# Performance work log

Measured on AMD Instinct MI355X. Metric: run time of the kernel, lower is better.

Reference implementation:

```python
import jax, jax.numpy as jnp
import numpy as np

T = 16000        # signal length
N1 = 120         # first-order filters (J=12, Q=10)
NPSI2 = 14       # second-order filterbank size (Q2=1)
NPAIR = 553      # second-order coefficients -> 120 + 553 = 673 channels
SUB1 = 8         # subsample U1 before order 2
T2 = T // SUB1   # 2000
STR1 = 1000      # lowpass stride at length T  -> 16 output samples
STR2 = T2 // (T // STR1)  # 125 -> 16 output samples
LOG_EPS = 1e-6
BN_EPS = 1e-5


def _gauss_hat(N, xi, sigma):
    om = np.arange(N) / N
    return np.exp(-((om - xi) ** 2) / (2.0 * sigma ** 2)).astype(np.float32)


def _filterbank():
    Q = 10.0
    xi1 = 0.45 * 2.0 ** (-np.arange(N1) / Q)
    sig1 = np.maximum(xi1 * 0.1, 2.0 / T)
    psi1 = np.stack([_gauss_hat(T, x, s) for x, s in zip(xi1, sig1)])
    phi1 = _gauss_hat(T, 0.0, 0.4 / STR1)
    xi2 = 0.45 * 2.0 ** (-np.arange(NPSI2, dtype=np.float64))
    sig2 = np.maximum(xi2 * 0.2, 2.0 / T2)
    psi2 = np.stack([_gauss_hat(T2, x, s) for x, s in zip(xi2, sig2)])
    phi2 = _gauss_hat(T2, 0.0, 0.4 / STR2)
    pairs = [(i, j) for i in range(N1) for j in range(NPSI2) if xi2[j] < xi1[i] / 2.0]
    pairs = pairs[:NPAIR]
    assert len(pairs) == NPAIR
    pi1 = np.array([p[0] for p in pairs], np.int32)
    pi2 = np.array([p[1] for p in pairs], np.int32)
    return psi1, phi1, psi2, phi2, pi1, pi2


def setup_inputs():
    key = jax.random.key(0)
    ks = jax.random.split(key, 8)
    psi1, phi1, psi2, phi2, pi1, pi2 = _filterbank()
    B = 32
    inp = {
        "x": jax.random.normal(ks[0], (B, 1, T), jnp.float32),
        "psi1_hat": jnp.asarray(psi1),
        "phi1_hat": jnp.asarray(phi1),
        "psi2_hat": jnp.asarray(psi2),
        "phi2_hat": jnp.asarray(phi2),
        "gamma": jnp.ones((673,), jnp.float32),
        "beta": jnp.zeros((673,), jnp.float32),
        "W1": jax.random.normal(ks[1], (300, 673), jnp.float32) * 0.04,
        "b1": jnp.zeros((300,), jnp.float32),
        "W2": jax.random.normal(ks[2], (90, 300), jnp.float32) * 0.06,
        "b2": jnp.zeros((90,), jnp.float32),
        "W3": jax.random.normal(ks[3], (35, 90), jnp.float32) * 0.1,
        "b3": jnp.zeros((35,), jnp.float32),
        "pair_i1": jnp.asarray(pi1),
        "pair_i2": jnp.asarray(pi2),
    }
    return inp


def reference(x, psi1_hat, phi1_hat, psi2_hat, phi2_hat, gamma, beta,
              W1, b1, W2, b2, W3, b3, pair_i1, pair_i2):
    xs = x.squeeze(1)                                       # [B, T]
    Xf = jnp.fft.fft(xs)                                    # [B, T] c64
    # --- order 1: wavelet conv (freq-domain), modulus ---
    U1 = jnp.abs(jnp.fft.ifft(Xf[:, None, :] * psi1_hat[None]))        # [B, N1, T]
    # S1 = lowpass(U1) subsampled to 16 samples
    S1 = jnp.real(jnp.fft.ifft(jnp.fft.fft(U1) * phi1_hat))[..., ::STR1]  # [B, N1, 16]
    # --- order 2 on subsampled U1 ---
    U1sf = jnp.fft.fft(U1[..., ::SUB1])                     # [B, N1, T2]
    U2 = jnp.abs(jnp.fft.ifft(U1sf[:, pair_i1, :] * psi2_hat[pair_i2]))  # [B, NPAIR, T2]
    S2 = jnp.real(jnp.fft.ifft(jnp.fft.fft(U2) * phi2_hat))[..., ::STR2]  # [B, NPAIR, 16]
    S = jnp.concatenate([S1, S2], axis=1)                   # [B, 673, 16]
    # log-abs + temporal mean pooling
    f = jnp.mean(jnp.log(jnp.abs(S) + LOG_EPS), axis=-1)    # [B, 673]
    # BatchNorm1d (training mode: batch statistics)
    mu = jnp.mean(f, axis=0)
    var = jnp.var(f, axis=0)
    f = (f - mu) / jnp.sqrt(var + BN_EPS) * gamma + beta
    # MLP head
    h = jax.nn.relu(f @ W1.T + b1)
    h = jax.nn.relu(h @ W2.T + b2)
    return jax.nn.log_softmax(h @ W3.T + b3, axis=-1)
```

## Files before the change

### kernel.cpp

```cpp
#include <hip/hip_runtime.h>
#include <math.h>

typedef float2 cf;

__device__ __forceinline__ cf cadd(cf a, cf b){ return make_float2(a.x+b.x, a.y+b.y); }
__device__ __forceinline__ cf csub(cf a, cf b){ return make_float2(a.x-b.x, a.y-b.y); }
__device__ __forceinline__ cf cmul(cf a, cf b){ return make_float2(a.x*b.x - a.y*b.y, a.x*b.y + a.y*b.x); }

__device__ __forceinline__ int SW(int i){ return i ^ ((i>>4)&15); }
#define AT(x) s[SW(x)]
#define WFENCE asm volatile("" ::: "memory")

template<bool WAVE> __device__ __forceinline__ void SYf(){
  if constexpr (WAVE) { WFENCE; } else __syncthreads();
}

__device__ __forceinline__ int devB(int i){
  int jm = i/10 + 2;
  double kc = 900.0*exp2((double)(-jm));
  double sg = fmax(180.0*exp2((double)(-jm)), 2.0);
  return min(2000, (int)ceil(kc + 6.5*sg) + 1);
}

template<int N, int L, bool INV>
__device__ __forceinline__ void stage_r2(cf* __restrict__ s, const cf* __restrict__ tw, int tid, int nt){
  constexpr int Ls = L/2, nbf = N/2, tws = 16000/L;
  for (int q = tid; q < nbf; q += nt){
    int blk = q / Ls, j = q - blk*Ls;
    int base = blk*L + j;
    cf w1 = tw[tws*j]; if (INV) w1.y = -w1.y;
    if (!INV){
      cf a = AT(base), b = AT(base+Ls);
      AT(base) = cadd(a,b);
      AT(base+Ls) = cmul(csub(a,b), w1);
    } else {
      cf a = AT(base), b = cmul(AT(base+Ls), w1);
      AT(base) = cadd(a,b);
      AT(base+Ls) = csub(a,b);
    }
  }
}

template<int N, int L, bool INV>
__device__ __forceinline__ void stage_r4(cf* __restrict__ s, const cf* __restrict__ tw, int tid, int nt){
  constexpr int Ls = L/4, nbf = N/4, tws = 16000/L;
  for (int q = tid; q < nbf; q += nt){
    int blk = q / Ls, j = q - blk*Ls;
    int base = blk*L + j;
    cf w1 = tw[tws*j]; if (INV) w1.y = -w1.y;
    cf w2 = cmul(w1,w1), w3 = cmul(w2,w1);
    if (!INV){
      cf y0=AT(base), y1=AT(base+Ls), y2=AT(base+2*Ls), y3=AT(base+3*Ls);
      cf t0=cadd(y0,y2), t1=csub(y0,y2), t2=cadd(y1,y3), t3=csub(y1,y3);
      AT(base)      = cadd(t0,t2);
      AT(base+Ls)   = cmul(make_float2(t1.x + t3.y, t1.y - t3.x), w1);
      AT(base+2*Ls) = cmul(csub(t0,t2), w2);
      AT(base+3*Ls) = cmul(make_float2(t1.x - t3.y, t1.y + t3.x), w3);
    } else {
      cf z0=AT(base);
      cf z1=cmul(AT(base+Ls),   w1);
      cf z2=cmul(AT(base+2*Ls), w2);
      cf z3=cmul(AT(base+3*Ls), w3);
      cf t0=cadd(z0,z2), t1=csub(z0,z2), t2=cadd(z1,z3), t3=csub(z1,z3);
      AT(base)      = cadd(t0,t2);
      AT(base+Ls)   = make_float2(t1.x - t3.y, t1.y + t3.x);
      AT(base+2*Ls) = csub(t0,t2);
      AT(base+3*Ls) = make_float2(t1.x + t3.y, t1.y - t3.x);
    }
  }
}

template<int N, int L, bool INV>
__device__ __forceinline__ void stage_r5(cf* __restrict__ s, const cf* __restrict__ tw, int tid, int nt){
  constexpr int Ls = L/5, nbf = N/5, tws = 16000/L;
  const float C1 = 0.30901699437494742f, S1c = 0.95105651629515357f;
  const float C2 = -0.80901699437494745f, S2c = 0.58778525229247314f;
  for (int q = tid; q < nbf; q += nt){
    int blk = q / Ls, j = q - blk*Ls;
    int base = blk*L + j;
    cf w1 = tw[tws*j]; if (INV) w1.y = -w1.y;
    cf w2 = cmul(w1,w1), w3 = cmul(w2,w1), w4 = cmul(w2,w2);
    if (!INV){
      cf y0=AT(base), y1=AT(base+Ls), y2=AT(base+2*Ls), y3=AT(base+3*Ls), y4=AT(base+4*Ls);
      cf t1=cadd(y1,y4), t2=csub(y1,y4), t3=cadd(y2,y3), t4=csub(y2,y3);
      cf z0 = cadd(y0, cadd(t1,t3));
      cf m1 = make_float2(y0.x + C1*t1.x + C2*t3.x, y0.y + C1*t1.y + C2*t3.y);
      cf m2 = make_float2(y0.x + C2*t1.x + C1*t3.x, y0.y + C2*t1.y + C1*t3.y);
      cf wa = make_float2(S1c*t2.x + S2c*t4.x, S1c*t2.y + S2c*t4.y);
      cf wb = make_float2(S2c*t2.x - S1c*t4.x, S2c*t2.y - S1c*t4.y);
      cf o1 = make_float2(m1.x + wa.y, m1.y - wa.x);
      cf o4 = make_float2(m1.x - wa.y, m1.y + wa.x);
      cf o2 = make_float2(m2.x + wb.y, m2.y - wb.x);
      cf o3 = make_float2(m2.x - wb.y, m2.y + wb.x);
      AT(base) = z0;
      AT(base+Ls)   = cmul(o1,w1);
      AT(base+2*Ls) = cmul(o2,w2);
      AT(base+3*Ls) = cmul(o3,w3);
      AT(base+4*Ls) = cmul(o4,w4);
    } else {
      cf z0=AT(base);
      cf z1=cmul(AT(base+Ls),   w1);
      cf z2=cmul(AT(base+2*Ls), w2);
      cf z3=cmul(AT(base+3*Ls), w3);
      cf z4=cmul(AT(base+4*Ls), w4);
      cf t1=cadd(z1,z4), t2=csub(z1,z4), t3=cadd(z2,z3), t4=csub(z2,z3);
      cf y0 = cadd(z0, cadd(t1,t3));
      cf m1 = make_float2(z0.x + C1*t1.x + C2*t3.x, z0.y + C1*t1.y + C2*t3.y);
      cf m2 = make_float2(z0.x + C2*t1.x + C1*t3.x, z0.y + C2*t1.y + C1*t3.y);
      cf wa = make_float2(S1c*t2.x + S2c*t4.x, S1c*t2.y + S2c*t4.y);
      cf wb = make_float2(S2c*t2.x - S1c*t4.x, S2c*t2.y - S1c*t4.y);
      AT(base)      = y0;
      AT(base+Ls)   = make_float2(m1.x - wa.y, m1.y + wa.x);
      AT(base+2*Ls) = make_float2(m2.x - wb.y, m2.y + wb.x);
      AT(base+3*Ls) = make_float2(m2.x + wb.y, m2.y - wb.x);
      AT(base+4*Ls) = make_float2(m1.x + wa.y, m1.y - wa.x);
    }
  }
}

template<bool INV>
__device__ void fft16000(cf* s, const cf* tw, int tid, int nt){
  if (!INV){
    stage_r5<16000,16000,false>(s,tw,tid,nt); __syncthreads();
    stage_r5<16000, 3200,false>(s,tw,tid,nt); __syncthreads();
    stage_r5<16000,  640,false>(s,tw,tid,nt); __syncthreads();
    stage_r4<16000,  128,false>(s,tw,tid,nt); __syncthreads();
    stage_r4<16000,   32,false>(s,tw,tid,nt); __syncthreads();
    stage_r4<16000,    8,false>(s,tw,tid,nt); __syncthreads();
    stage_r2<16000,    2,false>(s,tw,tid,nt); __syncthreads();
  } else {
    stage_r2<16000,    2,true >(s,tw,tid,nt); __syncthreads();
    stage_r4<16000,    8,true >(s,tw,tid,nt); __syncthreads();
    stage_r4<16000,   32,true >(s,tw,tid,nt); __syncthreads();
    stage_r4<16000,  128,true >(s,tw,tid,nt); __syncthreads();
    stage_r5<16000,  640,true >(s,tw,tid,nt); __syncthreads();
    stage_r5<16000, 3200,true >(s,tw,tid,nt); __syncthreads();
    stage_r5<16000,16000,true >(s,tw,tid,nt); __syncthreads();
  }
}

template<bool INV>
__device__ void fft2000(cf* s, const cf* tw, int tid, int nt){
  if (!INV){
    stage_r5<2000,2000,false>(s,tw,tid,nt); __syncthreads();
    stage_r5<2000, 400,false>(s,tw,tid,nt); __syncthreads();
    stage_r5<2000,  80,false>(s,tw,tid,nt); __syncthreads();
    stage_r4<2000,  16,false>(s,tw,tid,nt); __syncthreads();
    stage_r4<2000,   4,false>(s,tw,tid,nt); __syncthreads();
  } else {
    stage_r4<2000,   4,true >(s,tw,tid,nt); __syncthreads();
    stage_r4<2000,  16,true >(s,tw,tid,nt); __syncthreads();
    stage_r5<2000,  80,true >(s,tw,tid,nt); __syncthreads();
    stage_r5<2000, 400,true >(s,tw,tid,nt); __syncthreads();
    stage_r5<2000,2000,true >(s,tw,tid,nt); __syncthreads();
  }
}

__device__ void fft8000i(cf* s, const cf* tw, int tid, int nt){
  stage_r4<8000,   4,true>(s,tw,tid,nt); __syncthreads();
  stage_r4<8000,  16,true>(s,tw,tid,nt); __syncthreads();
  stage_r4<8000,  64,true>(s,tw,tid,nt); __syncthreads();
  stage_r5<8000, 320,true>(s,tw,tid,nt); __syncthreads();
  stage_r5<8000,1600,true>(s,tw,tid,nt); __syncthreads();
  stage_r5<8000,8000,true>(s,tw,tid,nt); __syncthreads();
}
__device__ void fft4000i(cf* s, const cf* tw, int tid, int nt){
  stage_r2<4000,   2,true>(s,tw,tid,nt); __syncthreads();
  stage_r4<4000,   8,true>(s,tw,tid,nt); __syncthreads();
  stage_r4<4000,  32,true>(s,tw,tid,nt); __syncthreads();
  stage_r5<4000, 160,true>(s,tw,tid,nt); __syncthreads();
  stage_r5<4000, 800,true>(s,tw,tid,nt); __syncthreads();
  stage_r5<4000,4000,true>(s,tw,tid,nt); __syncthreads();
}
__device__ void fft500i(cf* s, const cf* tw, int tid, int nt){
  stage_r4<500,  4,true>(s,tw,tid,nt); __syncthreads();
  stage_r5<500, 20,true>(s,tw,tid,nt); __syncthreads();
  stage_r5<500,100,true>(s,tw,tid,nt); __syncthreads();
  stage_r5<500,500,true>(s,tw,tid,nt); __syncthreads();
}
__device__ void fft1000i(cf* s, const cf* tw, int tid, int nt){
  stage_r2<1000,   2,true>(s,tw,tid,nt); __syncthreads();
  stage_r4<1000,   8,true>(s,tw,tid,nt); __syncthreads();
  stage_r5<1000,  40,true>(s,tw,tid,nt); __syncthreads();
  stage_r5<1000, 200,true>(s,tw,tid,nt); __syncthreads();
  stage_r5<1000,1000,true>(s,tw,tid,nt); __syncthreads();
}
__device__ __forceinline__ void fft250w(cf* s, const cf* tw, int lane){
  stage_r2<250,  2,true>(s,tw,lane,64); WFENCE;
  stage_r5<250, 10,true>(s,tw,lane,64); WFENCE;
  stage_r5<250, 50,true>(s,tw,lane,64); WFENCE;
  stage_r5<250,250,true>(s,tw,lane,64); WFENCE;
}

template<int M, bool INV, bool WAVE>
__device__ __forceinline__ void fftg(cf* s, const cf* tw, int tid, int nt){
  if constexpr (M==2000){
    if constexpr (INV){
      stage_r4<2000,4,true>(s,tw,tid,nt); SYf<WAVE>();
      stage_r4<2000,16,true>(s,tw,tid,nt); SYf<WAVE>();
      stage_r5<2000,80,true>(s,tw,tid,nt); SYf<WAVE>();
      stage_r5<2000,400,true>(s,tw,tid,nt); SYf<WAVE>();
      stage_r5<2000,2000,true>(s,tw,tid,nt); SYf<WAVE>();
    } else {
      stage_r5<2000,2000,false>(s,tw,tid,nt); SYf<WAVE>();
      stage_r5<2000,400,false>(s,tw,tid,nt); SYf<WAVE>();
      stage_r5<2000,80,false>(s,tw,tid,nt); SYf<WAVE>();
      stage_r4<2000,16,false>(s,tw,tid,nt); SYf<WAVE>();
      stage_r4<2000,4,false>(s,tw,tid,nt); SYf<WAVE>();
    }
  } else if constexpr (M==1600){
    if constexpr (INV){
      stage_r4<1600,4,true>(s,tw,tid,nt); SYf<WAVE>();
      stage_r4<1600,16,true>(s,tw,tid,nt); SYf<WAVE>();
      stage_r4<1600,64,true>(s,tw,tid,nt); SYf<WAVE>();
      stage_r5<1600,320,true>(s,tw,tid,nt); SYf<WAVE>();
      stage_r5<1600,1600,true>(s,tw,tid,nt); SYf<WAVE>();
    } else {
      stage_r5<1600,1600,false>(s,tw,tid,nt); SYf<WAVE>();
      stage_r5<1600,320,false>(s,tw,tid,nt); SYf<WAVE>();
      stage_r4<1600,64,false>(s,tw,tid,nt); SYf<WAVE>();
      stage_r4<1600,16,false>(s,tw,tid,nt); SYf<WAVE>();
      stage_r4<1600,4,false>(s,tw,tid,nt); SYf<WAVE>();
    }
  } else if constexpr (M==640){
    if constexpr (INV){
      stage_r2<640,2,true>(s,tw,tid,nt); SYf<WAVE>();
      stage_r4<640,8,true>(s,tw,tid,nt); SYf<WAVE>();
      stage_r4<640,32,true>(s,tw,tid,nt); SYf<WAVE>();
      stage_r4<640,128,true>(s,tw,tid,nt); SYf<WAVE>();
      stage_r5<640,640,true>(s,tw,tid,nt); SYf<WAVE>();
    } else {
      stage_r5<640,640,false>(s,tw,tid,nt); SYf<WAVE>();
      stage_r4<640,128,false>(s,tw,tid,nt); SYf<WAVE>();
      stage_r4<640,32,false>(s,tw,tid,nt); SYf<WAVE>();
      stage_r4<640,8,false>(s,tw,tid,nt); SYf<WAVE>();
      stage_r2<640,2,false>(s,tw,tid,nt); SYf<WAVE>();
    }
  } else if constexpr (M==320){
    if constexpr (INV){
      stage_r4<320,4,true>(s,tw,tid,nt); SYf<WAVE>();
      stage_r4<320,16,true>(s,tw,tid,nt); SYf<WAVE>();
      stage_r4<320,64,true>(s,tw,tid,nt); SYf<WAVE>();
      stage_r5<320,320,true>(s,tw,tid,nt); SYf<WAVE>();
    } else {
      stage_r5<320,320,false>(s,tw,tid,nt); SYf<WAVE>();
      stage_r4<320,64,false>(s,tw,tid,nt); SYf<WAVE>();
      stage_r4<320,16,false>(s,tw,tid,nt); SYf<WAVE>();
      stage_r4<320,4,false>(s,tw,tid,nt); SYf<WAVE>();
    }
  } else if constexpr (M==200){
    if constexpr (INV){
      stage_r2<200,2,true>(s,tw,tid,nt); SYf<WAVE>();
      stage_r4<200,8,true>(s,tw,tid,nt); SYf<WAVE>();
      stage_r5<200,40,true>(s,tw,tid,nt); SYf<WAVE>();
      stage_r5<200,200,true>(s,tw,tid,nt); SYf<WAVE>();
    } else {
      stage_r5<200,200,false>(s,tw,tid,nt); SYf<WAVE>();
      stage_r5<200,40,false>(s,tw,tid,nt); SYf<WAVE>();
      stage_r4<200,8,false>(s,tw,tid,nt); SYf<WAVE>();
      stage_r2<200,2,false>(s,tw,tid,nt); SYf<WAVE>();
    }
  } else {
    if constexpr (INV){
      stage_r2<160,2,true>(s,tw,tid,nt); SYf<WAVE>();
      stage_r4<160,8,true>(s,tw,tid,nt); SYf<WAVE>();
      stage_r4<160,32,true>(s,tw,tid,nt); SYf<WAVE>();
      stage_r5<160,160,true>(s,tw,tid,nt); SYf<WAVE>();
    } else {
      stage_r5<160,160,false>(s,tw,tid,nt); SYf<WAVE>();
      stage_r4<160,32,false>(s,tw,tid,nt); SYf<WAVE>();
      stage_r4<160,8,false>(s,tw,tid,nt); SYf<WAVE>();
      stage_r2<160,2,false>(s,tw,tid,nt); SYf<WAVE>();
    }
  }
}

__device__ __forceinline__ int pos16000(int k){
  int k0=k%5; k/=5; int k1=k%5; k/=5; int k2=k%5; k/=5;
  int k3=k&3; k>>=2; int k4=k&3; k>>=2; int k5=k&3; k>>=2;
  return k0*3200 + k1*640 + k2*128 + k3*32 + k4*8 + k5*2 + k;
}
__device__ __forceinline__ int pos8000(int k){
  int k0=k%5; k/=5; int k1=k%5; k/=5; int k2=k%5; k/=5;
  int k3=k&3, k4=(k>>2)&3, k5=k>>4;
  return k0*1600 + k1*320 + k2*64 + k3*16 + k4*4 + k5;
}
__device__ __forceinline__ int pos4000(int k){
  int k0=k%5; k/=5; int k1=k%5; k/=5; int k2=k%5; k/=5;
  int k3=k&3, k4=(k>>2)&3, k5=k>>4;
  return k0*800 + k1*160 + k2*32 + k3*8 + k4*2 + k5;
}
__device__ __forceinline__ int pos2000(int k){
  int k0=k%5; k/=5; int k1=k%5; k/=5; int k2=k%5; k/=5;
  int k3=k&3, k4=k>>2;
  return k0*400 + k1*80 + k2*16 + k3*4 + k4;
}
__device__ __forceinline__ int pos1600(int k){
  int k0=k%5; k/=5; int k1=k%5; k/=5;
  int k2=k&3; k>>=2; int k3=k&3; k>>=2;
  return k0*320 + k1*64 + k2*16 + k3*4 + k;
}
__device__ __forceinline__ int pos1000(int k){
  int k0=k%5; k/=5; int k1=k%5; k/=5; int k2=k%5; k/=5;
  int k3=k&3, k4=k>>2;
  return k0*200 + k1*40 + k2*8 + k3*2 + k4;
}
__device__ __forceinline__ int pos640(int k){
  int k0=k%5; k/=5;
  int k1=k&3; k>>=2; int k2=k&3; k>>=2; int k3=k&3; k>>=2;
  return k0*128 + k1*32 + k2*8 + k3*2 + k;
}
__device__ __forceinline__ int pos500(int k){
  int k0=k%5; k/=5; int k1=k%5; k/=5; int k2=k%5; k/=5;
  return k0*100 + k1*20 + k2*4 + k;
}
__device__ __forceinline__ int pos320(int k){
  int k0=k%5; k/=5;
  int k1=k&3; k>>=2; int k2=k&3; k>>=2;
  return k0*64 + k1*16 + k2*4 + k;
}
__device__ __forceinline__ int pos250(int k){
  int k0=k%5; k/=5; int k1=k%5; k/=5; int k2=k%5; k/=5;
  return k0*50 + k1*10 + k2*2 + k;
}
__device__ __forceinline__ int pos200(int k){
  int k0=k%5; k/=5; int k1=k%5; k/=5;
  int k2=k&3, k3=k>>2;
  return k0*40 + k1*8 + k2*2 + k3;
}
__device__ __forceinline__ int pos160(int k){
  int k0=k%5; k/=5;
  int k1=k&3; k>>=2; int k2=k&3; k>>=2;
  return k0*32 + k1*8 + k2*2 + k;
}

template<int M> __device__ __forceinline__ int posM(int k){
  if constexpr (M==8000) return pos8000(k);
  else if constexpr (M==4000) return pos4000(k);
  else return pos2000(k);
}
template<int M> __device__ __forceinline__ int posN(int k){
  if constexpr (M==2000) return pos2000(k);
  else if constexpr (M==1600) return pos1600(k);
  else if constexpr (M==640) return pos640(k);
  else if constexpr (M==320) return pos320(k);
  else if constexpr (M==200) return pos200(k);
  else return pos160(k);
}
template<int M> __device__ __forceinline__ void fftM_inv(cf* s, const cf* tw, int tid, int nt){
  if constexpr (M==8000) fft8000i(s,tw,tid,nt);
  else if constexpr (M==4000) fft4000i(s,tw,tid,nt);
  else fft2000<true>(s,tw,tid,nt);
}


__global__ void k_tw(cf* __restrict__ tw){
  int j = blockIdx.x*blockDim.x + threadIdx.x;
  if (j < 16000){
    double a = -6.283185307179586476925286766559 * (double)j / 16000.0;
    tw[j] = make_float2((float)cos(a), (float)sin(a));
  }
}

__global__ void k_btab(const float* __restrict__ phi1, const float* __restrict__ phi2,
                       float* __restrict__ h1g, float* __restrict__ h2g){
  int i = blockIdx.x*blockDim.x + threadIdx.x;
  const double TWO_PI = 6.283185307179586476925286766559;
  if (i < 5201){
    int d = i - 2600;
    double a = 0.0;
    for (int k = 0; k < 64; ++k) a += (double)phi1[k]*cos(TWO_PI*(double)(k*d)/16000.0);
    h1g[i] = (float)(a/16000.0 - (double)phi1[0]/32000.0);
  } else if (i == 5201){
    h1g[5201] = phi1[0]*(1.f/32000.f);
  } else if (i < 5202 + 661){
    int j = i - 5202; int d = j - 330;
    double a = 0.0;
    for (int k = 0; k < 64; ++k) a += (double)phi2[k]*cos(TWO_PI*(double)(k*d)/2000.0);
    h2g[j] = (float)(a/2000.0 - (double)phi2[0]/4000.0);
  } else if (i == 5202 + 661){
    h2g[661] = phi2[0]*(1.f/4000.f);
  }
}

__global__ __launch_bounds__(1024) void k_classify(const int* __restrict__ pi2,
                                                   int* __restrict__ list5, int* __restrict__ list4){
  __shared__ int w5[16], w4[16];
  int p = threadIdx.x;
  for (int t = p; t < 493; t += 1024) list5[t] = 0;
  for (int t = p; t < 60;  t += 1024) list4[t] = 0;
  bool valid = p < 553;
  int j2 = valid ? pi2[p] : 99;
  bool f5 = valid && (j2 >= 5);
  bool f4 = valid && (j2 < 5);
  unsigned long long m5 = __ballot(f5);
  unsigned long long m4 = __ballot(f4);
  int lane = p & 63, wid = p >> 6;
  if (lane == 0){ w5[wid] = __popcll(m5); w4[wid] = __popcll(m4); }
  __syncthreads();
  if (valid){
    int b5 = 0, b4 = 0;
    for (int w = 0; w < wid; ++w){ b5 += w5[w]; b4 += w4[w]; }
    unsigned long long lm = (1ull << lane) - 1ull;
    if (f5) list5[b5 + __popcll(m5 & lm)] = p;
    if (f4) list4[b4 + __popcll(m4 & lm)] = p;
  }
}

__global__ __launch_bounds__(1024) void k_fftx(const float* __restrict__ x, cf* __restrict__ Xf,
                                               const cf* __restrict__ tw){
  extern __shared__ cf s[];
  int b = blockIdx.x;
  int tid = threadIdx.x, nt = blockDim.x;
  for (int n = tid; n < 16000; n += nt) AT(n) = make_float2(x[b*16000 + n], 0.f);
  __syncthreads();
  fft16000<false>(s, tw, tid, nt);
  for (int k = tid; k < 16000; k += nt) Xf[b*16000 + k] = AT(pos16000(k));
}

template<int PR, int NF, int I0>
__global__ __launch_bounds__(1024) void kf16(const cf* __restrict__ Xf, const float* __restrict__ psi1,
                                             const float* __restrict__ h1g, const cf* __restrict__ tw,
                                             cf* __restrict__ U1sf, float* __restrict__ S1){
  extern __shared__ cf s[];
  float* part = (float*)(s + 8000);
  int b = blockIdx.x / NF;
  int i = I0 + (blockIdx.x - b*NF);
  int tid = threadIdx.x, wid = tid>>6, lane = tid&63;
  double x1 = 0.45 * exp2((double)(-i)/10.0);
  double kc = 16000.0*x1, sg = fmax(1600.0*x1, 2.0);
  int k0 = max(0,(int)floor(kc-6.5*sg));
  int k1 = min(16000,(int)ceil(kc+6.5*sg)+1);
  const cf* X = Xf + (size_t)b*16000;
  const float* P = psi1 + (size_t)i*16000;
  for (int j = tid; j < 8000; j += 1024){
    cf acc = make_float2(0.f,0.f);
    if (j >= k0 && j < k1){ cf v = X[j]; float pf = P[j]; acc.x = v.x*pf; acc.y = v.y*pf; }
    int j2 = j + 8000;
    if (j2 >= k0 && j2 < k1){
      cf v = X[j2]; float pf = P[j2];
      if (PR==0){ acc.x += v.x*pf; acc.y += v.y*pf; } else { acc.x -= v.x*pf; acc.y -= v.y*pf; }
    }
    if (PR==1){ cf ph = tw[j]; ph.y = -ph.y; acc = cmul(acc, ph); }
    AT(pos8000(j)) = acc;
  }
  __syncthreads();
  fft8000i(s, tw, tid, 1024);
  float mreg[8]; float tsum = 0.f;
  #pragma unroll
  for (int r = 0; r < 8; ++r){
    int n = tid + (r<<10);
    cf v = AT(n);
    mreg[r] = sqrtf(v.x*v.x+v.y*v.y)*(1.f/16000.f);
    tsum += mreg[r];
  }
  float* fl = (float*)s;
  __syncthreads();
  #pragma unroll
  for (int r = 0; r < 8; ++r) fl[tid + (r<<10)] = mreg[r];
  #pragma unroll
  for (int o = 32; o > 0; o >>= 1) tsum += __shfl_xor(tsum, o);
  if (lane == 0) part[wid] = tsum;
  __syncthreads();
  if (tid == 0){ float tt = 0.f; for (int w = 0; w < 16; ++w) tt += part[w]; part[16] = tt; }
  __syncthreads();
  float stot = part[16];
  float c1 = h1g[5201];
  {
    int t = wid;
    float acc = 0.f;
    if (PR == 0){
      for (int u = -1300 + lane; u <= 1300; u += 64){
        int m = 500*t - u;
        if (m < 0) m += 8000; else if (m >= 8000) m -= 8000;
        acc = fmaf(fl[m], h1g[2*u + 2600], acc);
      }
    } else {
      for (int u = -1300 + lane; u <= 1299; u += 64){
        int m = 500*t - u - 1;
        if (m < 0) m += 8000; else if (m >= 8000) m -= 8000;
        acc = fmaf(fl[m], h1g[2*u + 2601], acc);
      }
    }
    #pragma unroll
    for (int o = 32; o > 0; o >>= 1) acc += __shfl_xor(acc, o);
    if (lane == 0){
      float val = acc + c1*stot;
      size_t idx = ((size_t)b*120 + i)*16 + t;
      if (PR == 0) S1[idx] = val; else S1[idx] += val;
    }
  }
  if constexpr (PR == 0){
    cf* s2 = s + 4000;
    __syncthreads();
    for (int q = tid; q < 2000; q += 1024) s2[SW(q)] = make_float2(fl[4*q], 0.f);
    __syncthreads();
    fft2000<false>(s2, tw, tid, 1024);
    int B = devB(i);
    cf* out = U1sf + ((size_t)b*120 + i)*2000;
    for (int k = tid; k < B; k += 1024) out[k] = s2[SW(pos2000(k))];
  }
}

template<int M, int ST, int NF, int I0, int NT>
__global__ __launch_bounds__(NT) void kf(const cf* __restrict__ Xf, const float* __restrict__ psi1,
                                         const float* __restrict__ h1g, const cf* __restrict__ tw,
                                         cf* __restrict__ U1sf, float* __restrict__ S1){
  extern __shared__ cf s[];
  constexpr int NW = NT/64;
  int b = blockIdx.x / NF;
  int i = I0 + (blockIdx.x - b*NF);
  int tid = threadIdx.x, wid = tid>>6, lane = tid&63;
  double x1 = 0.45 * exp2((double)(-i) / 10.0);
  double kc = 16000.0 * x1;
  double sg = fmax(1600.0 * x1, 2.0);
  int k0 = max(0, (int)floor(kc - 6.5*sg));
  int k1 = min(16000, (int)ceil(kc + 6.5*sg) + 1);
  int W = k1 - k0;
  for (int n = tid; n < M; n += NT) s[n] = make_float2(0.f, 0.f);
  __syncthreads();
  const cf* X = Xf + (size_t)b*16000 + k0;
  const float* P = psi1 + (size_t)i*16000 + k0;
  for (int j = tid; j < W; j += NT){
    cf v = X[j]; float pf = P[j];
    int pp = posM<M>(j);
    AT(pp) = make_float2(v.x*pf, v.y*pf);
  }
  __syncthreads();
  fftM_inv<M>(s, tw, tid, NT);
  constexpr int R = (M + NT - 1)/NT;
  float mreg[R]; float tsum = 0.f;
  const float inv = 1.f/16000.f;
  #pragma unroll
  for (int r = 0; r < R; ++r){
    int n = tid + r*NT;
    if (n < M){ cf v = AT(n); mreg[r] = sqrtf(v.x*v.x + v.y*v.y)*inv; tsum += mreg[r]; }
    else mreg[r] = 0.f;
  }
  float* fl = (float*)s;
  float* part = (float*)(s + M);
  __syncthreads();
  #pragma unroll
  for (int r = 0; r < R; ++r){ int n = tid + r*NT; if (n < M) fl[n] = mreg[r]; }
  #pragma unroll
  for (int o = 32; o > 0; o >>= 1) tsum += __shfl_xor(tsum, o);
  if (lane == 0) part[wid] = tsum;
  __syncthreads();
  if (tid == 0){ float tt = 0.f; for (int w = 0; w < NW; ++w) tt += part[w]; part[NW] = tt; }
  __syncthreads();
  float stot = part[NW];
  float c1 = h1g[5201];
  for (int t = wid; t < 16; t += NW){
    int mlo = (1000*t - 2600)/ST;
    int mhi = (1000*t + 2600)/ST;
    float acc = 0.f;
    for (int m = mlo + lane; m <= mhi; m += 64){
      int mm = m; if (mm < 0) mm += M; else if (mm >= M) mm -= M;
      acc = fmaf(fl[mm], h1g[1000*t - m*ST + 2600], acc);
    }
    #pragma unroll
    for (int o = 32; o > 0; o >>= 1) acc += __shfl_xor(acc, o);
    if (lane == 0) S1[((size_t)b*120 + i)*16 + t] = (float)ST*(acc + c1*stot);
  }
  constexpr int K = 8/ST;
  float d0 = fl[tid*K];
  float d1 = 0.f;
  { int m2 = tid + 1024; if (m2 < 2000) d1 = fl[m2*K]; }
  __syncthreads();
  AT(tid) = make_float2(d0, 0.f);
  { int m2 = tid + 1024; if (m2 < 2000) AT(m2) = make_float2(d1, 0.f); }
  __syncthreads();
  fft2000<false>(s, tw, tid, NT);
  int B = devB(i);
  cf* out = U1sf + ((size_t)b*120 + i)*2000;
  for (int k = tid; k < B; k += NT) out[k] = AT(pos2000(k));
}

template<int M, int NF, int I0>
__global__ __launch_bounds__(256) void k_n2(const cf* __restrict__ Xf, const float* __restrict__ psi1,
                                            const float* __restrict__ phi1, const cf* __restrict__ tw,
                                            cf* __restrict__ U1sf, float* __restrict__ S1){
  extern __shared__ cf s[];
  int b = blockIdx.x / NF;
  int i = I0 + (blockIdx.x - b*NF);
  int tid = threadIdx.x, wid = tid>>6, lane = tid&63;
  double x1 = 0.45 * exp2((double)(-i)/10.0);
  double kc = 16000.0*x1, sg = fmax(1600.0*x1, 2.0);
  int k0 = max(0,(int)floor(kc-6.5*sg));
  int k1 = min(16000,(int)ceil(kc+6.5*sg)+1);
  int W = k1-k0;
  for (int n = tid; n < M; n += 256) s[n] = make_float2(0.f,0.f);
  __syncthreads();
  const cf* X = Xf + (size_t)b*16000 + k0;
  const float* P = psi1 + (size_t)i*16000 + k0;
  for (int j = tid; j < W; j += 256){
    cf v = X[j]; float pf = P[j];
    AT(posN<M>(j)) = make_float2(v.x*pf, v.y*pf);
  }
  __syncthreads();
  fftg<M,true,false>(s,tw,tid,256);
  for (int n = tid; n < M; n += 256){
    cf v = AT(n);
    AT(n) = make_float2(sqrtf(v.x*v.x+v.y*v.y)*(1.f/16000.f), 0.f);
  }
  __syncthreads();
  fftg<M,false,false>(s,tw,tid,256);
  {
    int k = lane;
    cf g = AT(posN<M>(k));
    float ph = phi1[k];
    float gx = g.x*ph, gy = g.y*ph;
    float* S1o = S1 + ((size_t)b*120+i)*16;
    for (int r = 0; r < 4; ++r){
      int t = wid + 4*r;
      cf e = tw[1000*((k*t)&15)];
      float val = gx*e.x + gy*e.y;
      #pragma unroll
      for (int o = 32; o > 0; o >>= 1) val += __shfl_xor(val, o);
      if (lane == 0) S1o[t] = val*(1.f/(float)M);
    }
  }
  int B = devB(i);
  const float sc = 2000.f/(float)M;
  cf* out = U1sf + ((size_t)b*120+i)*2000;
  for (int k = tid; k < B; k += 256){
    cf v = AT(posN<M>(k));
    out[k] = make_float2(v.x*sc, v.y*sc);
  }
}

template<int M, int SPAD, int NF, int I0, int WPB>
__global__ __launch_bounds__(WPB*64) void k_nw2(const cf* __restrict__ Xf, const float* __restrict__ psi1,
                                                const float* __restrict__ phi1, const cf* __restrict__ tw,
                                                cf* __restrict__ U1sf, float* __restrict__ S1){
  extern __shared__ cf sh[];
  int wid = threadIdx.x >> 6, lane = threadIdx.x & 63;
  int q = blockIdx.x*WPB + wid;
  int filt = q >> 5, b = q & 31;
  int i = I0 + filt;
  cf* s = sh + wid*SPAD;
  double x1 = 0.45 * exp2((double)(-i)/10.0);
  double kc = 16000.0*x1, sg = fmax(1600.0*x1, 2.0);
  int k0 = max(0,(int)floor(kc-6.5*sg));
  int k1 = min(16000,(int)ceil(kc+6.5*sg)+1);
  int W = k1-k0;
  for (int n = lane; n < SPAD; n += 64) s[n] = make_float2(0.f,0.f);
  WFENCE;
  const cf* X = Xf + (size_t)b*16000 + k0;
  const float* P = psi1 + (size_t)i*16000 + k0;
  for (int j = lane; j < W; j += 64){
    cf v = X[j]; float pf = P[j];
    AT(posN<M>(j)) = make_float2(v.x*pf, v.y*pf);
  }
  WFENCE;
  fftg<M,true,true>(s,tw,lane,64);
  for (int n = lane; n < M; n += 64){
    cf v = AT(n);
    AT(n) = make_float2(sqrtf(v.x*v.x+v.y*v.y)*(1.f/16000.f), 0.f);
  }
  WFENCE;
  fftg<M,false,true>(s,tw,lane,64);
  {
    int k = lane;
    cf g = AT(posN<M>(k));
    float ph = phi1[k];
    float gx = g.x*ph, gy = g.y*ph;
    float* S1o = S1 + ((size_t)b*120+i)*16;
    for (int t = 0; t < 16; ++t){
      cf e = tw[1000*((k*t)&15)];
      float val = gx*e.x + gy*e.y;
      #pragma unroll
      for (int o = 32; o > 0; o >>= 1) val += __shfl_xor(val, o);
      if (lane == 0) S1o[t] = val*(1.f/(float)M);
    }
  }
  int B = devB(i);
  const float sc = 2000.f/(float)M;
  cf* out = U1sf + ((size_t)b*120+i)*2000;
  for (int k = lane; k < B; k += 64){
    cf v = AT(posN<M>(k));
    out[k] = make_float2(v.x*sc, v.y*sc);
  }
}

__global__ __launch_bounds__(256) void k_sec5(const cf* __restrict__ U1sf, const float* __restrict__ psi2,
                                              const float* __restrict__ h2g, const cf* __restrict__ tw,
                                              const int* __restrict__ pi1, const int* __restrict__ pi2,
                                              const int* __restrict__ list5, float* __restrict__ S2){
  __shared__ cf sall[4*256];
  __shared__ float flall[4*256];
  int wid = threadIdx.x >> 6, lane = threadIdx.x & 63;
  int q = blockIdx.x*4 + wid;
  int p = list5[q >> 5];
  int b = q & 31;
  int i1 = pi1[p], j2 = pi2[p];
  cf* s = sall + wid*256;
  float* fl2 = flall + wid*256;
  double xc = exp2((double)(-j2));
  double kc = 900.0*xc, sg = fmax(180.0*xc, 2.0);
  int k0 = max(0, (int)floor(kc - 6.5*sg));
  int k1 = min(2000, (int)ceil(kc + 6.5*sg) + 1);
  int W = k1 - k0;
  for (int n = lane; n < 256; n += 64) s[n] = make_float2(0.f, 0.f);
  WFENCE;
  const cf* U = U1sf + (size_t)(b*120 + i1)*2000 + k0;
  const float* F = psi2 + j2*2000 + k0;
  for (int j = lane; j < W; j += 64){
    cf v = U[j]; float f = F[j];
    AT(pos250(j)) = make_float2(v.x*f, v.y*f);
  }
  WFENCE;
  fft250w(s, tw, lane);
  float tsum = 0.f;
  #pragma unroll
  for (int r = 0; r < 4; ++r){
    int n = lane + r*64;
    if (n < 250){
      cf v = AT(n);
      float mg = sqrtf(v.x*v.x + v.y*v.y)*(1.f/2000.f);
      fl2[n] = mg; tsum += mg;
    }
  }
  WFENCE;
  #pragma unroll
  for (int o = 32; o > 0; o >>= 1) tsum += __shfl_xor(tsum, o);
  float stot = tsum;
  float c2 = h2g[661];
  float* S2o = S2 + (size_t)(b*553 + p)*16;
  for (int t = 0; t < 16; ++t){
    int mlo = (125*t - 330 + 7) >> 3;
    int mhi = (125*t + 330) >> 3;
    float acc = 0.f;
    for (int m = mlo + lane; m <= mhi; m += 64){
      int mm = m; if (mm < 0) mm += 250; else if (mm >= 250) mm -= 250;
      acc = fmaf(fl2[mm], h2g[125*t - m*8 + 330], acc);
    }
    #pragma unroll
    for (int o = 32; o > 0; o >>= 1) acc += __shfl_xor(acc, o);
    if (lane == 0) S2o[t] = 8.f*(acc + c2*stot);
  }
}

__global__ __launch_bounds__(128) void k_secbig(const cf* __restrict__ U1sf, const float* __restrict__ psi2,
                                                const float* __restrict__ h2g, const cf* __restrict__ tw,
                                                const int* __restrict__ pi1, const int* __restrict__ pi2,
                                                const int* __restrict__ list4, float* __restrict__ S2){
  extern __shared__ cf s[];
  float* fl2 = (float*)(s + 2000);
  float* part = fl2 + 2000;
  int p = list4[blockIdx.x >> 5];
  int b = blockIdx.x & 31;
  int tid = threadIdx.x, wid = tid>>6, lane = tid&63;
  int i1 = pi1[p], j2 = pi2[p];
  int M2, s2l;
  if (j2 == 4){ M2 = 500;  s2l = 2; }
  else if (j2 == 3){ M2 = 1000; s2l = 1; }
  else { M2 = 2000; s2l = 0; }
  int ST2 = 1 << s2l;
  double xc = exp2((double)(-j2));
  double kc = 900.0*xc, sg = fmax(180.0*xc, 2.0);
  int k0 = max(0, (int)floor(kc - 6.5*sg));
  int k1 = min(2000, (int)ceil(kc + 6.5*sg) + 1);
  int W = k1 - k0;
  int M2r = (M2 + 15) & ~15;
  for (int n = tid; n < M2r; n += 128) s[n] = make_float2(0.f, 0.f);
  __syncthreads();
  const cf* U = U1sf + (size_t)(b*120 + i1)*2000 + k0;
  const float* F = psi2 + j2*2000 + k0;
  for (int j = tid; j < W; j += 128){
    cf v = U[j]; float f = F[j];
    int pp;
    if (M2 == 500) pp = pos500(j);
    else if (M2 == 1000) pp = pos1000(j);
    else pp = pos2000(j);
    AT(pp) = make_float2(v.x*f, v.y*f);
  }
  __syncthreads();
  if (M2 == 500) fft500i(s, tw, tid, 128);
  else if (M2 == 1000) fft1000i(s, tw, tid, 128);
  else fft2000<true>(s, tw, tid, 128);
  float tsum = 0.f;
  for (int n = tid; n < M2; n += 128){
    cf v = AT(n);
    float mg = sqrtf(v.x*v.x + v.y*v.y)*(1.f/2000.f);
    fl2[n] = mg; tsum += mg;
  }
  #pragma unroll
  for (int o = 32; o > 0; o >>= 1) tsum += __shfl_xor(tsum, o);
  if (lane == 0) part[wid] = tsum;
  __syncthreads();
  float stot = part[0] + part[1];
  float c2 = h2g[661];
  float* S2o = S2 + (size_t)(b*553 + p)*16;
  for (int r = 0; r < 8; ++r){
    int t = wid + (r<<1);
    int mlo = (125*t - 330 + ST2 - 1) >> s2l;
    int mhi = (125*t + 330) >> s2l;
    float acc = 0.f;
    for (int m = mlo + lane; m <= mhi; m += 64){
      int mm = m; if (mm < 0) mm += M2; else if (mm >= M2) mm -= M2;
      acc = fmaf(fl2[mm], h2g[125*t - m*ST2 + 330], acc);
    }
    #pragma unroll
    for (int o = 32; o > 0; o >>= 1) acc += __shfl_xor(acc, o);
    if (lane == 0) S2o[t] = (float)ST2*(acc + c2*stot);
  }
}

__global__ __launch_bounds__(64) void k_fbn(const float* __restrict__ S1, const float* __restrict__ S2,
                                            const float* __restrict__ g, const float* __restrict__ be,
                                            float* __restrict__ fn){
  int j = blockIdx.x;
  int b = threadIdx.x;
  float f = 0.f;
  if (b < 32){
    const float* src = (j < 120) ? (S1 + (b*120 + j)*16) : (S2 + (b*553 + (j-120))*16);
    float acc = 0.f;
    #pragma unroll
    for (int t = 0; t < 16; ++t) acc += logf(fabsf(src[t]) + 1e-6f);
    f = acc * (1.f/16.f);
  }
  float mu = f;
  #pragma unroll
  for (int o = 16; o > 0; o >>= 1) mu += __shfl_xor(mu, o);
  mu *= (1.f/32.f);
  float d = f - mu;
  float v = d*d;
  #pragma unroll
  for (int o = 16; o > 0; o >>= 1) v += __shfl_xor(v, o);
  v *= (1.f/32.f);
  float is = g[j] / sqrtf(v + 1e-5f);
  if (b < 32) fn[b*673 + j] = d*is + be[j];
}

__global__ __launch_bounds__(512) void k_mlp1(const float* __restrict__ fn,
                                              const float* __restrict__ W1, const float* __restrict__ b1,
                                              float* __restrict__ h1o){
  int task = blockIdx.x*8 + (threadIdx.x >> 6);
  int lane = threadIdx.x & 63;
  if (task >= 32*300) return;
  int b = task / 300, r = task - b*300;
  const float* f = fn + b*673;
  const float* w = W1 + r*673;
  float acc = 0.f;
  for (int k = lane; k < 673; k += 64) acc = fmaf(f[k], w[k], acc);
  #pragma unroll
  for (int o = 32; o > 0; o >>= 1) acc += __shfl_down(acc, o);
  if (lane == 0) h1o[b*300 + r] = fmaxf(acc + b1[r], 0.f);
}

__global__ __launch_bounds__(512) void k_mlp2(const float* __restrict__ h1,
                                              const float* __restrict__ W2, const float* __restrict__ b2,
                                              float* __restrict__ h2o){
  int task = blockIdx.x*8 + (threadIdx.x >> 6);
  int lane = threadIdx.x & 63;
  if (task >= 32*90) return;
  int b = task / 90, r = task - b*90;
  const float* h = h1 + b*300;
  const float* w = W2 + r*300;
  float acc = 0.f;
  for (int k = lane; k < 300; k += 64) acc = fmaf(h[k], w[k], acc);
  #pragma unroll
  for (int o = 32; o > 0; o >>= 1) acc += __shfl_down(acc, o);
  if (lane == 0) h2o[b*90 + r] = fmaxf(acc + b2[r], 0.f);
}

__global__ __launch_bounds__(256) void k_mlp3(const float* __restrict__ h2,
                                              const float* __restrict__ W3, const float* __restrict__ b3,
                                              float* __restrict__ out){
  __shared__ float lg[35];
  int b = blockIdx.x;
  int tid = threadIdx.x, wid = tid >> 6, lane = tid & 63;
  for (int r = wid; r < 35; r += 4){
    float acc = 0.f;
    for (int k = lane; k < 90; k += 64) acc = fmaf(h2[b*90 + k], W3[r*90 + k], acc);
    #pragma unroll
    for (int o = 32; o > 0; o >>= 1) acc += __shfl_down(acc, o);
    if (lane == 0) lg[r] = acc + b3[r];
  }
  __syncthreads();
  if (tid < 64){
    float v = (tid < 35) ? lg[tid] : -1e30f;
    float mx = v;
    #pragma unroll
    for (int o = 32; o > 0; o >>= 1) mx = fmaxf(mx, __shfl_xor(mx, o));
    float e = (tid < 35) ? expf(v - mx) : 0.f;
    float se = e;
    #pragma unroll
    for (int o = 32; o > 0; o >>= 1) se += __shfl_xor(se, o);
    if (tid < 35) out[b*35 + tid] = v - mx - logf(se);
  }
}


extern "C" void kernel_launch(void* const* d_in, const int* in_sizes, int n_in,
                              void* d_out, int out_size, void* d_ws, size_t ws_size,
                              hipStream_t stream){
  const float* x     = (const float*)d_in[0];
  const float* psi1  = (const float*)d_in[1];
  const float* phi1  = (const float*)d_in[2];
  const float* psi2  = (const float*)d_in[3];
  const float* phi2  = (const float*)d_in[4];
  const float* gamma = (const float*)d_in[5];
  const float* beta  = (const float*)d_in[6];
  const float* W1    = (const float*)d_in[7];
  const float* b1    = (const float*)d_in[8];
  const float* W2    = (const float*)d_in[9];
  const float* b2    = (const float*)d_in[10];
  const float* W3    = (const float*)d_in[11];
  const float* b3    = (const float*)d_in[12];
  const int*   pi1   = (const int*)d_in[13];
  const int*   pi2   = (const int*)d_in[14];

  char* ws = (char*)d_ws;
  constexpr size_t o_tw = 0;
  constexpr size_t o_Xf = o_tw + (size_t)16000*sizeof(cf);
  constexpr size_t o_U  = o_Xf + (size_t)32*16000*sizeof(cf);
  constexpr size_t o_S1 = o_U  + (size_t)3840*2000*sizeof(cf);
  constexpr size_t o_S2 = o_S1 + (size_t)3840*16*sizeof(float);
  constexpr size_t o_l5 = o_S2 + (size_t)17696*16*sizeof(float);
  constexpr size_t o_l4 = o_l5 + (size_t)512*sizeof(int);
  constexpr size_t o_fn = o_l4 + (size_t)64*sizeof(int);
  constexpr size_t o_h1 = o_fn + (size_t)32*673*sizeof(float);
  constexpr size_t o_h2 = o_h1 + (size_t)5202*sizeof(float);
  constexpr size_t o_m1 = o_h2 + (size_t)662*sizeof(float);
  constexpr size_t o_m2 = o_m1 + (size_t)32*300*sizeof(float);

  cf*    tw    = (cf*)(ws + o_tw);
  cf*    Xf    = (cf*)(ws + o_Xf);
  cf*    U1sf  = (cf*)(ws + o_U);
  float* S1b   = (float*)(ws + o_S1);
  float* S2b   = (float*)(ws + o_S2);
  int*   list5 = (int*)(ws + o_l5);
  int*   list4 = (int*)(ws + o_l4);
  float* fnbuf = (float*)(ws + o_fn);
  float* h1g   = (float*)(ws + o_h1);
  float* h2g   = (float*)(ws + o_h2);
  float* m1buf = (float*)(ws + o_m1);
  float* m2buf = (float*)(ws + o_m2);

  hipFuncSetAttribute((const void*)k_fftx, hipFuncAttributeMaxDynamicSharedMemorySize, 131072);

  k_tw<<<63, 256, 0, stream>>>(tw);
  k_btab<<<23, 256, 0, stream>>>(phi1, phi2, h1g, h2g);
  k_classify<<<1, 1024, 0, stream>>>(pi2, list5, list4);
  k_fftx<<<32, 1024, 128000, stream>>>(x, Xf, tw);
  kf16<0,13,0><<<32*13, 1024, 8000*8 + 17*4, stream>>>(Xf, psi1, h1g, tw, U1sf, S1b);
  kf16<1,13,0><<<32*13, 1024, 8000*8 + 17*4, stream>>>(Xf, psi1, h1g, tw, U1sf, S1b);
  kf< 8000,2,10,13,1024><<<32*10, 1024,  8000*8 + 17*4, stream>>>(Xf, psi1, h1g, tw, U1sf, S1b);
  kf< 4000,4,10,23,1024><<<32*10, 1024,  4000*8 + 17*4, stream>>>(Xf, psi1, h1g, tw, U1sf, S1b);
  k_n2<2000,10,33><<<32*10, 256, 2000*8, stream>>>(Xf, psi1, phi1, tw, U1sf, S1b);
  k_n2<1600,10,43><<<32*10, 256, 1600*8, stream>>>(Xf, psi1, phi1, tw, U1sf, S1b);
  k_nw2<640,640,10,53,4><<< 80, 256, 4*640*8, stream>>>(Xf, psi1, phi1, tw, U1sf, S1b);
  k_nw2<320,320,10,63,8><<< 40, 512, 8*320*8, stream>>>(Xf, psi1, phi1, tw, U1sf, S1b);
  k_nw2<200,208,10,73,8><<< 40, 512, 8*208*8, stream>>>(Xf, psi1, phi1, tw, U1sf, S1b);
  k_nw2<160,160,37,83,8><<<148, 512, 8*160*8, stream>>>(Xf, psi1, phi1, tw, U1sf, S1b);
  k_sec5<<<(493*32)/4, 256, 0, stream>>>(U1sf, psi2, h2g, tw, pi1, pi2, list5, S2b);
  k_secbig<<<60*32, 128, 2000*8 + 2000*4 + 4*4, stream>>>(U1sf, psi2, h2g, tw, pi1, pi2, list4, S2b);
  k_fbn<<<673, 64, 0, stream>>>(S1b, S2b, gamma, beta, fnbuf);
  k_mlp1<<<1200, 512, 0, stream>>>(fnbuf, W1, b1, m1buf);
  k_mlp2<<<360, 512, 0, stream>>>(m1buf, W2, b2, m2buf);
  k_mlp3<<<32, 256, 0, stream>>>(m2buf, W3, b3, (float*)d_out);
}
```

Baseline: 394.5 us.

## Merge split-half order-1 kernels, shrink second-order FFT, spread lowpass over lanes

The two templated order-1 kernels that handled the even and odd half-spectrum are merged into one launch with twice the blocks. The parity is now taken from the block index, and the odd half writes its S1 partial to a separate buffer that the BN kernel adds back in. This removes a launch and the serial dependency between the two halves. In the second-order small kernel, filters with j2>=6 now use a 125-point inverse FFT instead of 250 with a rescaled lowpass stride, and the 16 lowpass outputs are computed by groups of 16 lanes instead of looping over t with full-wave reductions. Runtime branches replace compile-time ones, which may cost registers or add divergence.

```diff
diff --git a/kernel.cpp b/kernel.cpp
--- a/kernel.cpp
+++ b/kernel.cpp
@@ -191,6 +191,11 @@
   stage_r5<250, 50,true>(s,tw,lane,64); WFENCE;
   stage_r5<250,250,true>(s,tw,lane,64); WFENCE;
 }
+__device__ __forceinline__ void fft125w(cf* s, const cf* tw, int lane){
+  stage_r5<125,  5,true>(s,tw,lane,64); WFENCE;
+  stage_r5<125, 25,true>(s,tw,lane,64); WFENCE;
+  stage_r5<125,125,true>(s,tw,lane,64); WFENCE;
+}
 
 template<int M, bool INV, bool WAVE>
 __device__ __forceinline__ void fftg(cf* s, const cf* tw, int tid, int nt){
@@ -322,6 +327,10 @@
 __device__ __forceinline__ int pos250(int k){
   int k0=k%5; k/=5; int k1=k%5; k/=5; int k2=k%5; k/=5;
   return k0*50 + k1*10 + k2*2 + k;
+}
+__device__ __forceinline__ int pos125(int k){
+  int k0=k%5; k/=5; int k1=k%5; k/=5;
+  return k0*25 + k1*5 + k;
 }
 __device__ __forceinline__ int pos200(int k){
   int k0=k%5; k/=5; int k1=k%5; k/=5;
@@ -418,14 +427,18 @@
   for (int k = tid; k < 16000; k += nt) Xf[b*16000 + k] = AT(pos16000(k));
 }
 
-template<int PR, int NF, int I0>
-__global__ __launch_bounds__(1024) void kf16(const cf* __restrict__ Xf, const float* __restrict__ psi1,
-                                             const float* __restrict__ h1g, const cf* __restrict__ tw,
-                                             cf* __restrict__ U1sf, float* __restrict__ S1){
+template<int NF, int I0>
+__global__ __launch_bounds__(1024) void kf16c(const cf* __restrict__ Xf, const float* __restrict__ psi1,
+                                              const float* __restrict__ h1g, const cf* __restrict__ tw,
+                                              cf* __restrict__ U1sf, float* __restrict__ S1,
+                                              float* __restrict__ S1o){
   extern __shared__ cf s[];
   float* part = (float*)(s + 8000);
-  int b = blockIdx.x / NF;
-  int i = I0 + (blockIdx.x - b*NF);
+  int q = blockIdx.x;
+  int pr = q & 1;
+  int rest = q >> 1;
+  int b = rest / NF;
+  int i = I0 + (rest - b*NF);
   int tid = threadIdx.x, wid = tid>>6, lane = tid&63;
   double x1 = 0.45 * exp2((double)(-i)/10.0);
   double kc = 16000.0*x1, sg = fmax(1600.0*x1, 2.0);
@@ -439,9 +452,9 @@
     int j2 = j + 8000;
     if (j2 >= k0 && j2 < k1){
       cf v = X[j2]; float pf = P[j2];
-      if (PR==0){ acc.x += v.x*pf; acc.y += v.y*pf; } else { acc.x -= v.x*pf; acc.y -= v.y*pf; }
-    }
-    if (PR==1){ cf ph = tw[j]; ph.y = -ph.y; acc = cmul(acc, ph); }
+      if (pr==0){ acc.x += v.x*pf; acc.y += v.y*pf; } else { acc.x -= v.x*pf; acc.y -= v.y*pf; }
+    }
+    if (pr==1){ cf ph = tw[j]; ph.y = -ph.y; acc = cmul(acc, ph); }
     AT(pos8000(j)) = acc;
   }
   __syncthreads();
@@ -469,7 +482,7 @@
   {
     int t = wid;
     float acc = 0.f;
-    if (PR == 0){
+    if (pr == 0){
       for (int u = -1300 + lane; u <= 1300; u += 64){
         int m = 500*t - u;
         if (m < 0) m += 8000; else if (m >= 8000) m -= 8000;
@@ -486,14 +499,14 @@
     for (int o = 32; o > 0; o >>= 1) acc += __shfl_xor(acc, o);
     if (lane == 0){
       float val = acc + c1*stot;
-      size_t idx = ((size_t)b*120 + i)*16 + t;
-      if (PR == 0) S1[idx] = val; else S1[idx] += val;
-    }
-  }
-  if constexpr (PR == 0){
+      if (pr == 0) S1[((size_t)b*120 + i)*16 + t] = val;
+      else         S1o[((size_t)b*NF + (i - I0))*16 + t] = val;
+    }
+  }
+  if (pr == 0){
     cf* s2 = s + 4000;
     __syncthreads();
-    for (int q = tid; q < 2000; q += 1024) s2[SW(q)] = make_float2(fl[4*q], 0.f);
+    for (int qq = tid; qq < 2000; qq += 1024) s2[SW(qq)] = make_float2(fl[4*qq], 0.f);
     __syncthreads();
     fft2000<false>(s2, tw, tid, 1024);
     int B = devB(i);
@@ -696,6 +709,8 @@
   int i1 = pi1[p], j2 = pi2[p];
   cf* s = sall + wid*256;
   float* fl2 = flall + wid*256;
+  int M2  = (j2 >= 6) ? 125 : 250;
+  int s2l = (j2 >= 6) ? 4 : 3;
   double xc = exp2((double)(-j2));
   double kc = 900.0*xc, sg = fmax(180.0*xc, 2.0);
   int k0 = max(0, (int)floor(kc - 6.5*sg));
@@ -707,15 +722,16 @@
   const float* F = psi2 + j2*2000 + k0;
   for (int j = lane; j < W; j += 64){
     cf v = U[j]; float f = F[j];
-    AT(pos250(j)) = make_float2(v.x*f, v.y*f);
+    int pp = (M2 == 125) ? pos125(j) : pos250(j);
+    AT(pp) = make_float2(v.x*f, v.y*f);
   }
   WFENCE;
-  fft250w(s, tw, lane);
+  if (M2 == 125) fft125w(s, tw, lane); else fft250w(s, tw, lane);
   float tsum = 0.f;
   #pragma unroll
   for (int r = 0; r < 4; ++r){
     int n = lane + r*64;
-    if (n < 250){
+    if (n < M2){
       cf v = AT(n);
       float mg = sqrtf(v.x*v.x + v.y*v.y)*(1.f/2000.f);
       fl2[n] = mg; tsum += mg;
@@ -726,18 +742,22 @@
   for (int o = 32; o > 0; o >>= 1) tsum += __shfl_xor(tsum, o);
   float stot = tsum;
   float c2 = h2g[661];
+  float scale = (float)(1 << s2l);
   float* S2o = S2 + (size_t)(b*553 + p)*16;
-  for (int t = 0; t < 16; ++t){
-    int mlo = (125*t - 330 + 7) >> 3;
-    int mhi = (125*t + 330) >> 3;
+  int g16 = lane >> 4, li = lane & 15;
+  for (int r = 0; r < 4; ++r){
+    int t = g16*4 + r;
+    int x0 = 125*t - 330, x1b = 125*t + 330;
+    int mlo = (x0 + ((1<<s2l)-1)) >> s2l;
+    int mhi = x1b >> s2l;
     float acc = 0.f;
-    for (int m = mlo + lane; m <= mhi; m += 64){
-      int mm = m; if (mm < 0) mm += 250; else if (mm >= 250) mm -= 250;
-      acc = fmaf(fl2[mm], h2g[125*t - m*8 + 330], acc);
+    for (int m = mlo + li; m <= mhi; m += 16){
+      int mm = m; if (mm < 0) mm += M2; else if (mm >= M2) mm -= M2;
+      acc = fmaf(fl2[mm], h2g[125*t - (m << s2l) + 330], acc);
     }
     #pragma unroll
-    for (int o = 32; o > 0; o >>= 1) acc += __shfl_xor(acc, o);
-    if (lane == 0) S2o[t] = 8.f*(acc + c2*stot);
+    for (int o = 8; o > 0; o >>= 1) acc += __shfl_xor(acc, o);
+    if (li == 0) S2o[t] = scale*(acc + c2*stot);
   }
 }
 
@@ -807,17 +827,30 @@
   }
 }
 
-__global__ __launch_bounds__(64) void k_fbn(const float* __restrict__ S1, const float* __restrict__ S2,
+__global__ __launch_bounds__(64) void k_fbn(const float* __restrict__ S1, const float* __restrict__ S1o,
+                                            const float* __restrict__ S2,
                                             const float* __restrict__ g, const float* __restrict__ be,
                                             float* __restrict__ fn){
   int j = blockIdx.x;
   int b = threadIdx.x;
   float f = 0.f;
   if (b < 32){
-    const float* src = (j < 120) ? (S1 + (b*120 + j)*16) : (S2 + (b*553 + (j-120))*16);
     float acc = 0.f;
-    #pragma unroll
-    for (int t = 0; t < 16; ++t) acc += logf(fabsf(src[t]) + 1e-6f);
+    if (j < 120){
+      const float* src = S1 + (b*120 + j)*16;
+      if (j < 13){
+        const float* srco = S1o + (b*13 + j)*16;
+        #pragma unroll
+        for (int t = 0; t < 16; ++t) acc += logf(fabsf(src[t] + srco[t]) + 1e-6f);
+      } else {
+        #pragma unroll
+        for (int t = 0; t < 16; ++t) acc += logf(fabsf(src[t]) + 1e-6f);
+      }
+    } else {
+      const float* src = S2 + (b*553 + (j-120))*16;
+      #pragma unroll
+      for (int t = 0; t < 16; ++t) acc += logf(fabsf(src[t]) + 1e-6f);
+    }
     f = acc * (1.f/16.f);
   }
   float mu = f;
@@ -925,6 +958,7 @@
   constexpr size_t o_h2 = o_h1 + (size_t)5202*sizeof(float);
   constexpr size_t o_m1 = o_h2 + (size_t)662*sizeof(float);
   constexpr size_t o_m2 = o_m1 + (size_t)32*300*sizeof(float);
+  constexpr size_t o_so = o_m2 + (size_t)32*90*sizeof(float);
 
   cf*    tw    = (cf*)(ws + o_tw);
   cf*    Xf    = (cf*)(ws + o_Xf);
@@ -938,15 +972,17 @@
   float* h2g   = (float*)(ws + o_h2);
   float* m1buf = (float*)(ws + o_m1);
   float* m2buf = (float*)(ws + o_m2);
+  float* S1ob  = (float*)(ws + o_so);
 
   hipFuncSetAttribute((const void*)k_fftx, hipFuncAttributeMaxDynamicSharedMemorySize, 131072);
+  hipFuncSetAttribute((const void*)kf16c<13,0>, hipFuncAttributeMaxDynamicSharedMemorySize, 131072);
+  hipFuncSetAttribute((const void*)kf< 8000,2,10,13,1024>, hipFuncAttributeMaxDynamicSharedMemorySize, 131072);
 
   k_tw<<<63, 256, 0, stream>>>(tw);
   k_btab<<<23, 256, 0, stream>>>(phi1, phi2, h1g, h2g);
   k_classify<<<1, 1024, 0, stream>>>(pi2, list5, list4);
   k_fftx<<<32, 1024, 128000, stream>>>(x, Xf, tw);
-  kf16<0,13,0><<<32*13, 1024, 8000*8 + 17*4, stream>>>(Xf, psi1, h1g, tw, U1sf, S1b);
-  kf16<1,13,0><<<32*13, 1024, 8000*8 + 17*4, stream>>>(Xf, psi1, h1g, tw, U1sf, S1b);
+  kf16c<13,0><<<32*13*2, 1024, 8000*8 + 17*4, stream>>>(Xf, psi1, h1g, tw, U1sf, S1b, S1ob);
   kf< 8000,2,10,13,1024><<<32*10, 1024,  8000*8 + 17*4, stream>>>(Xf, psi1, h1g, tw, U1sf, S1b);
   kf< 4000,4,10,23,1024><<<32*10, 1024,  4000*8 + 17*4, stream>>>(Xf, psi1, h1g, tw, U1sf, S1b);
   k_n2<2000,10,33><<<32*10, 256, 2000*8, stream>>>(Xf, psi1, phi1, tw, U1sf, S1b);
@@ -957,7 +993,7 @@
   k_nw2<160,160,37,83,8><<<148, 512, 8*160*8, stream>>>(Xf, psi1, phi1, tw, U1sf, S1b);
   k_sec5<<<(493*32)/4, 256, 0, stream>>>(U1sf, psi2, h2g, tw, pi1, pi2, list5, S2b);
   k_secbig<<<60*32, 128, 2000*8 + 2000*4 + 4*4, stream>>>(U1sf, psi2, h2g, tw, pi1, pi2, list4, S2b);
-  k_fbn<<<673, 64, 0, stream>>>(S1b, S2b, gamma, beta, fnbuf);
+  k_fbn<<<673, 64, 0, stream>>>(S1b, S1ob, S2b, gamma, beta, fnbuf);
   k_mlp1<<<1200, 512, 0, stream>>>(fnbuf, W1, b1, m1buf);
   k_mlp2<<<360, 512, 0, stream>>>(m1buf, W2, b2, m2buf);
   k_mlp3<<<32, 256, 0, stream>>>(m2buf, W3, b3, (float*)d_out);
```

Measured after the change: 380.1 us. 3.6% less time.
